# Optimization experiments

Measured on AMD Instinct MI355X. Metric: run time of the kernel, lower is better.

Reference implementation:

```python
import jax, jax.numpy as jnp
import numpy as np

B, F, H, W = 2, 512, 192, 192
T = 8
NEAR, FAR = 0.5, 100.0
EPS = 1e-8


def setup_inputs() -> dict:
    key = jax.random.key(0)
    k1, k2, k3, k4, k5 = jax.random.split(key, 5)
    # triangles in NDC: xy in [-1,1], z (depth) in [NEAR, FAR)
    center = jax.random.uniform(k1, (B, F, 1, 2), minval=-0.9, maxval=0.9)
    offset = jax.random.uniform(k2, (B, F, 3, 2), minval=-0.15, maxval=0.15)
    xy = center + offset                                      # [B,F,3,2]
    z = (jax.random.uniform(k3, (B, F, 1, 1), minval=2.0, maxval=8.0)
         + jax.random.uniform(k5, (B, F, 3, 1), minval=0.0, maxval=0.2))
    faces = jnp.concatenate([xy, z], axis=-1)                 # [B,F,3,3]
    textures = jax.random.normal(k4, (B, F, 3, T))            # per-vertex features
    return {"faces": faces, "textures": textures}


def _rasterize_maps(faces):
    # faces: [B,F,3,3] -> face_index_map [B,H,W] int32, weight_map [B,H,W,3], depth_map [B,H,W]
    dt = faces.dtype
    px = ((2.0 * (jnp.arange(W, dtype=dt) + 0.5) - W) / W)[None, None, None, :]  # [1,1,1,W]
    py = ((2.0 * (jnp.arange(H, dtype=dt) + 0.5) - H) / H)[None, None, :, None]  # [1,1,H,1]
    x = faces[..., 0][..., None, None]  # [B,F,3,1,1]
    y = faces[..., 1][..., None, None]
    z = faces[..., 2][..., None, None]
    x0, x1, x2 = x[:, :, 0], x[:, :, 1], x[:, :, 2]  # [B,F,1,1]
    y0, y1, y2 = y[:, :, 0], y[:, :, 1], y[:, :, 2]
    z0, z1, z2 = z[:, :, 0], z[:, :, 1], z[:, :, 2]
    det = (x1 - x0) * (y2 - y0) - (x2 - x0) * (y1 - y0)
    ok = jnp.abs(det) > EPS
    inv_det = jnp.where(ok, det, 1.0)
    inv_det = 1.0 / inv_det
    # screen-space barycentric weights, [B,F,H,W]
    w0 = ((x1 - px) * (y2 - py) - (x2 - px) * (y1 - py)) * inv_det
    w1 = ((x2 - px) * (y0 - py) - (x0 - px) * (y2 - py)) * inv_det
    w2 = 1.0 - w0 - w1
    inside = (w0 >= 0.0) & (w1 >= 0.0) & (w2 >= 0.0) & ok
    # perspective-correct depth: 1 / sum_k w_k / z_k
    inv_depth = w0 / z0 + w1 / z1 + w2 / z2
    depth = jnp.where(inv_depth > EPS, 1.0 / jnp.maximum(inv_depth, EPS), FAR)
    valid = inside & (depth >= NEAR) & (depth <= FAR)
    cand = jnp.where(valid, depth, FAR)            # [B,F,H,W]
    best = jnp.argmin(cand, axis=1)                # z-buffer winner, [B,H,W]
    take = lambda a: jnp.take_along_axis(a, best[:, None], axis=1)[:, 0]
    min_depth = take(cand)
    covered = min_depth < FAR
    face_index_map = jnp.where(covered, best, -1).astype(jnp.int32)
    weight_map = jnp.where(covered[..., None],
                           jnp.stack([take(w0), take(w1), take(w2)], axis=-1), 0.0)
    depth_map = jnp.where(covered, min_depth, FAR)
    return face_index_map, weight_map, depth_map


def reference(faces, textures):
    fim, wmap, dmap = _rasterize_maps(faces)
    Bp = faces.shape[0]
    idx = jnp.maximum(fim, 0).reshape(Bp, H * W)
    # gather winning face's per-vertex features: [B,HW,3,T]
    tex = jnp.take_along_axis(textures, idx[:, :, None, None], axis=1)
    feat = jnp.einsum('bpk,bpkt->bpt', wmap.reshape(Bp, H * W, 3), tex).reshape(Bp, H, W, T)
    mask = (fim >= 0).astype(feat.dtype)[..., None]
    feature_map = jnp.concatenate([feat, mask], axis=-1)   # [B,H,W,T+1]
    feature = jnp.transpose(feature_map, (0, 3, 1, 2))     # [B,T+1,H,W]
    return feature, fim, dmap
```

## Files before the change

### kernel.cpp

```cpp
#include <hip/hip_runtime.h>
#include <hip/hip_bf16.h>


namespace {
constexpr int BB = 2, FF = 512, HH = 192, WW = 192, TT = 8;
constexpr int TILE = 16;
constexpr int HWSZ = HH * WW;
constexpr float NEARF = 0.5f, FARF = 100.0f, EPSF = 1e-8f;
}

__global__ __launch_bounds__(256) void raster_fused_kernel(
    const float* __restrict__ faces,
    const float* __restrict__ textures,
    float* __restrict__ out)
{
#pragma clang fp contract(off)
  __shared__ float sx0[FF], sy0[FF], sx1[FF], sy1[FF], sx2[FF], sy2[FF];
  __shared__ float siz0[FF], siz1[FF], siz2[FF], sinv[FF];
  __shared__ int s_count;
  __shared__ unsigned short s_list[FF];

  const int tx = threadIdx.x, ty = threadIdx.y;
  const int tid = ty * TILE + tx;
  const int bx = blockIdx.x, by = blockIdx.y, b = blockIdx.z;

  if (tid == 0) s_count = 0;
  __syncthreads();

  const float px_lo = (2.0f * ((float)(bx * TILE) + 0.5f) - (float)WW) / (float)WW;
  const float px_hi = (2.0f * ((float)(bx * TILE + TILE - 1) + 0.5f) - (float)WW) / (float)WW;
  const float py_lo = (2.0f * ((float)(by * TILE) + 0.5f) - (float)HH) / (float)HH;
  const float py_hi = (2.0f * ((float)(by * TILE + TILE - 1) + 0.5f) - (float)HH) / (float)HH;

  for (int f = tid; f < FF; f += 256) {
    const float* fp = faces + (size_t)(b * FF + f) * 9;
    float x0 = fp[0], y0 = fp[1], z0 = fp[2];
    float x1 = fp[3], y1 = fp[4], z1 = fp[5];
    float x2 = fp[6], y2 = fp[7], z2 = fp[8];
    float det = (x1 - x0) * (y2 - y0) - (x2 - x0) * (y1 - y0);
    bool ok = fabsf(det) > EPSF;
    float invdet = 1.0f / (ok ? det : 1.0f);
    sx0[f] = x0; sy0[f] = y0;
    sx1[f] = x1; sy1[f] = y1;
    sx2[f] = x2; sy2[f] = y2;
    siz0[f] = 1.0f / z0; siz1[f] = 1.0f / z1; siz2[f] = 1.0f / z2;
    sinv[f] = invdet;
    if (ok) {
      float xmn = fminf(x0, fminf(x1, x2)), xmx = fmaxf(x0, fmaxf(x1, x2));
      float ymn = fminf(y0, fminf(y1, y2)), ymx = fmaxf(y0, fmaxf(y1, y2));
      if (xmx >= px_lo && xmn <= px_hi && ymx >= py_lo && ymn <= py_hi) {
        int slot = atomicAdd(&s_count, 1);
        s_list[slot] = (unsigned short)f;
      }
    }
  }
  __syncthreads();

  const int w = bx * TILE + tx;
  const int h = by * TILE + ty;
  const float px = (2.0f * ((float)w + 0.5f) - (float)WW) / (float)WW;
  const float py = (2.0f * ((float)h + 0.5f) - (float)HH) / (float)HH;

  float best = FARF;
  int bestf = 0;
  float bw0 = 0.0f, bw1 = 0.0f, bw2 = 0.0f;
  const int cnt = s_count;
  for (int i = 0; i < cnt; ++i) {
    const int f = s_list[i];
    float dx0 = sx0[f] - px, dy0 = sy0[f] - py;
    float dx1 = sx1[f] - px, dy1 = sy1[f] - py;
    float dx2 = sx2[f] - px, dy2 = sy2[f] - py;
    float invdet = sinv[f];
    float w0 = (dx1 * dy2 - dx2 * dy1) * invdet;
    float w1 = (dx2 * dy0 - dx0 * dy2) * invdet;
    float w2 = 1.0f - w0 - w1;
    if (w0 >= 0.0f && w1 >= 0.0f && w2 >= 0.0f) {
      float invd = w0 * siz0[f] + w1 * siz1[f] + w2 * siz2[f];
      if (invd > EPSF) {
        float d = 1.0f / invd;
        if (d >= NEARF && d <= FARF && d < best) {
          best = d; bestf = f;
          bw0 = w0; bw1 = w1; bw2 = w2;
        }
      }
    }
  }

  const bool covered = best < FARF;
  const size_t pix = (size_t)h * WW + w;
  float* featp = out + (size_t)b * 9 * HWSZ + pix;
  if (covered) {
    const float* tp = textures + (size_t)(b * FF + bestf) * 3 * TT;
    #pragma unroll
    for (int t = 0; t < TT; ++t) {
      float v0 = tp[t];
      float v1 = tp[TT + t];
      float v2 = tp[2 * TT + t];
      float v = bw0 * v0 + bw1 * v1;
      v = v + bw2 * v2;
      featp[(size_t)t * HWSZ] = v;
    }
    featp[(size_t)TT * HWSZ] = 1.0f;
  } else {
    #pragma unroll
    for (int t = 0; t < TT + 1; ++t) featp[(size_t)t * HWSZ] = 0.0f;
  }

  const size_t fim_base = (size_t)BB * 9 * HWSZ;
  const size_t dmap_base = fim_base + (size_t)BB * HWSZ;
  out[fim_base + (size_t)b * HWSZ + pix] = covered ? (float)bestf : -1.0f;
  out[dmap_base + (size_t)b * HWSZ + pix] = best;
}

extern "C" void kernel_launch(void* const* d_in, const int* in_sizes, int n_in,
                              void* d_out, int out_size, void* d_ws, size_t ws_size,
                              hipStream_t stream) {
  const float* faces = (const float*)d_in[0];
  const float* textures = (const float*)d_in[1];
  float* out = (float*)d_out;
  dim3 grid(WW / TILE, HH / TILE, BB);
  dim3 block(TILE, TILE, 1);
  hipLaunchKernelGGL(raster_fused_kernel, grid, block, 0, stream,
                     faces, textures, out);
}
```

Measured before the change: 63.32 us.

## Pack per-face data as AoS in LDS, stage faces via float4, prefetch next face

Each block first copies its batch's raw face array into shared memory with float4 loads. The per-face setup data is then packed into a 12-float array-of-structs record, so the inner loop fetches one face with two float4 reads and one float2 read instead of ten scalar reads. The next face's record is software-prefetched into registers, and texture rows are fetched as float4 vectors. This adds about 18KB of extra LDS, which could reduce occupancy, and adds register pressure from the prefetch.

```diff
diff --git a/kernel.cpp b/kernel.cpp
--- a/kernel.cpp
+++ b/kernel.cpp
@@ -6,6 +6,7 @@
 constexpr int BB = 2, FF = 512, HH = 192, WW = 192, TT = 8;
 constexpr int TILE = 16;
 constexpr int HWSZ = HH * WW;
+constexpr int RAW = FF * 9;
 constexpr float NEARF = 0.5f, FARF = 100.0f, EPSF = 1e-8f;
 }
 
@@ -15,8 +16,8 @@
     float* __restrict__ out)
 {
 #pragma clang fp contract(off)
-  __shared__ float sx0[FF], sy0[FF], sx1[FF], sy1[FF], sx2[FF], sy2[FF];
-  __shared__ float siz0[FF], siz1[FF], siz2[FF], sinv[FF];
+  __shared__ float sraw[RAW];
+  __shared__ float sface[FF * 12];
   __shared__ int s_count;
   __shared__ unsigned short s_list[FF];
 
@@ -25,6 +26,12 @@
   const int bx = blockIdx.x, by = blockIdx.y, b = blockIdx.z;
 
   if (tid == 0) s_count = 0;
+
+  {
+    const float4* src = (const float4*)(faces + (size_t)b * RAW);
+    float4* dst = (float4*)sraw;
+    for (int i = tid; i < RAW / 4; i += 256) dst[i] = src[i];
+  }
   __syncthreads();
 
   const float px_lo = (2.0f * ((float)(bx * TILE) + 0.5f) - (float)WW) / (float)WW;
@@ -33,18 +40,17 @@
   const float py_hi = (2.0f * ((float)(by * TILE + TILE - 1) + 0.5f) - (float)HH) / (float)HH;
 
   for (int f = tid; f < FF; f += 256) {
-    const float* fp = faces + (size_t)(b * FF + f) * 9;
+    const float* fp = sraw + f * 9;
     float x0 = fp[0], y0 = fp[1], z0 = fp[2];
     float x1 = fp[3], y1 = fp[4], z1 = fp[5];
     float x2 = fp[6], y2 = fp[7], z2 = fp[8];
     float det = (x1 - x0) * (y2 - y0) - (x2 - x0) * (y1 - y0);
     bool ok = fabsf(det) > EPSF;
     float invdet = 1.0f / (ok ? det : 1.0f);
-    sx0[f] = x0; sy0[f] = y0;
-    sx1[f] = x1; sy1[f] = y1;
-    sx2[f] = x2; sy2[f] = y2;
-    siz0[f] = 1.0f / z0; siz1[f] = 1.0f / z1; siz2[f] = 1.0f / z2;
-    sinv[f] = invdet;
+    float* dst = sface + f * 12;
+    dst[0] = x0; dst[1] = y0; dst[2] = x1; dst[3] = y1;
+    dst[4] = x2; dst[5] = y2; dst[6] = invdet; dst[7] = 1.0f / z0;
+    dst[8] = 1.0f / z1; dst[9] = 1.0f / z2;
     if (ok) {
       float xmn = fminf(x0, fminf(x1, x2)), xmx = fmaxf(x0, fmaxf(x1, x2));
       float ymn = fminf(y0, fminf(y1, y2)), ymx = fmaxf(y0, fmaxf(y1, y2));
@@ -65,22 +71,35 @@
   int bestf = 0;
   float bw0 = 0.0f, bw1 = 0.0f, bw2 = 0.0f;
   const int cnt = s_count;
-  for (int i = 0; i < cnt; ++i) {
-    const int f = s_list[i];
-    float dx0 = sx0[f] - px, dy0 = sy0[f] - py;
-    float dx1 = sx1[f] - px, dy1 = sy1[f] - py;
-    float dx2 = sx2[f] - px, dy2 = sy2[f] - py;
-    float invdet = sinv[f];
-    float w0 = (dx1 * dy2 - dx2 * dy1) * invdet;
-    float w1 = (dx2 * dy0 - dx0 * dy2) * invdet;
-    float w2 = 1.0f - w0 - w1;
-    if (w0 >= 0.0f && w1 >= 0.0f && w2 >= 0.0f) {
-      float invd = w0 * siz0[f] + w1 * siz1[f] + w2 * siz2[f];
-      if (invd > EPSF) {
-        float d = 1.0f / invd;
-        if (d >= NEARF && d <= FARF && d < best) {
-          best = d; bestf = f;
-          bw0 = w0; bw1 = w1; bw2 = w2;
+
+  if (cnt > 0) {
+    int fnext = s_list[0];
+    float4 r0 = *(const float4*)(sface + fnext * 12);
+    float4 r1 = *(const float4*)(sface + fnext * 12 + 4);
+    float2 r2 = *(const float2*)(sface + fnext * 12 + 8);
+    for (int i = 0; i < cnt; ++i) {
+      const float4 c0 = r0; const float4 c1 = r1; const float2 c2 = r2;
+      const int fcur = fnext;
+      if (i + 1 < cnt) {
+        fnext = s_list[i + 1];
+        r0 = *(const float4*)(sface + fnext * 12);
+        r1 = *(const float4*)(sface + fnext * 12 + 4);
+        r2 = *(const float2*)(sface + fnext * 12 + 8);
+      }
+      float dx0 = c0.x - px, dy0 = c0.y - py;
+      float dx1 = c0.z - px, dy1 = c0.w - py;
+      float dx2 = c1.x - px, dy2 = c1.y - py;
+      float w0 = (dx1 * dy2 - dx2 * dy1) * c1.z;
+      float w1 = (dx2 * dy0 - dx0 * dy2) * c1.z;
+      float w2 = 1.0f - w0 - w1;
+      if (w0 >= 0.0f && w1 >= 0.0f && w2 >= 0.0f) {
+        float invd = w0 * c1.w + w1 * c2.x + w2 * c2.y;
+        if (invd > EPSF) {
+          float d = 1.0f / invd;
+          if (d >= NEARF && d <= FARF && d < best) {
+            best = d; bestf = fcur;
+            bw0 = w0; bw1 = w1; bw2 = w2;
+          }
         }
       }
     }
@@ -90,14 +109,19 @@
   const size_t pix = (size_t)h * WW + w;
   float* featp = out + (size_t)b * 9 * HWSZ + pix;
   if (covered) {
-    const float* tp = textures + (size_t)(b * FF + bestf) * 3 * TT;
+    const float4* tp = (const float4*)(textures + (size_t)(b * FF + bestf) * 3 * TT);
+    float4 t0 = tp[0], t1 = tp[1];
+    float4 t2 = tp[2], t3 = tp[3];
+    float4 t4 = tp[4], t5 = tp[5];
+    const float* v0 = (const float*)&t0;
+    float a0[8] = {t0.x, t0.y, t0.z, t0.w, t1.x, t1.y, t1.z, t1.w};
+    float a1[8] = {t2.x, t2.y, t2.z, t2.w, t3.x, t3.y, t3.z, t3.w};
+    float a2[8] = {t4.x, t4.y, t4.z, t4.w, t5.x, t5.y, t5.z, t5.w};
+    (void)v0;
     #pragma unroll
     for (int t = 0; t < TT; ++t) {
-      float v0 = tp[t];
-      float v1 = tp[TT + t];
-      float v2 = tp[2 * TT + t];
-      float v = bw0 * v0 + bw1 * v1;
-      v = v + bw2 * v2;
+      float v = bw0 * a0[t] + bw1 * a1[t];
+      v = v + bw2 * a2[t];
       featp[(size_t)t * HWSZ] = v;
     }
     featp[(size_t)TT * HWSZ] = 1.0f;
```

New measurement: 62.65 us. No clear change (-1.1%).
